# Kernel optimization log

Hardware: AMD Instinct MI355X
Metric: run time of the kernel (lower is better)

## Reference

```python
import jax, jax.numpy as jnp
import numpy as np

D_MODEL = 1024
NHEAD = 16
HEAD_DIM = D_MODEL // NHEAD
D_FF = 4096
B, S = 2, 2048
LN_EPS = 1e-5


def _linear_params(key, d_out, d_in):
    kw, kb = jax.random.split(key)
    lim = 1.0 / np.sqrt(d_in)
    W = jax.random.uniform(kw, (d_out, d_in), jnp.float32, -lim, lim)
    b = jax.random.uniform(kb, (d_out,), jnp.float32, -lim, lim)
    return W, b


def setup_inputs() -> dict:
    key = jax.random.key(0)
    ks = jax.random.split(key, 8)
    src = jax.random.normal(ks[0], (B, S, D_MODEL), jnp.float32)
    mask = jax.random.randint(ks[1], (B, S), 0, 2).astype(bool)
    Wq, bq = _linear_params(ks[2], D_MODEL, D_MODEL)
    Wk, bk = _linear_params(ks[3], D_MODEL, D_MODEL)
    Wv, bv = _linear_params(ks[4], D_MODEL, D_MODEL)
    Wo, bo = _linear_params(ks[5], D_MODEL, D_MODEL)
    W1, b1 = _linear_params(ks[6], D_FF, D_MODEL)
    W2, b2 = _linear_params(ks[7], D_MODEL, D_FF)
    ln1_g = jnp.ones((D_MODEL,), jnp.float32)
    ln1_b = jnp.zeros((D_MODEL,), jnp.float32)
    ln2_g = jnp.ones((D_MODEL,), jnp.float32)
    ln2_b = jnp.zeros((D_MODEL,), jnp.float32)
    return dict(src=src, mask=mask, Wq=Wq, bq=bq, Wk=Wk, bk=bk, Wv=Wv, bv=bv,
                Wo=Wo, bo=bo, W1=W1, b1=b1, W2=W2, b2=b2,
                ln1_g=ln1_g, ln1_b=ln1_b, ln2_g=ln2_g, ln2_b=ln2_b)


def _layernorm(x, g, b):
    mu = jnp.mean(x, axis=-1, keepdims=True)
    var = jnp.mean(jnp.square(x - mu), axis=-1, keepdims=True)
    return (x - mu) * jax.lax.rsqrt(var + LN_EPS) * g + b


def reference(src, mask, Wq, bq, Wk, bk, Wv, bv, Wo, bo, W1, b1, W2, b2,
              ln1_g, ln1_b, ln2_g, ln2_b):
    batch, seq, _ = src.shape
    src_norm = _layernorm(src, ln1_g, ln1_b)
    # projections (torch Linear: x @ W.T + b), split heads -> [B,H,S,Dh]
    def proj(W, b):
        y = jnp.einsum('bsi,oi->bso', src_norm, W) + b
        return y.reshape(batch, seq, NHEAD, HEAD_DIM).transpose(0, 2, 1, 3)
    q, k, v = proj(Wq, bq), proj(Wk, bk), proj(Wv, bv)
    scores = jnp.einsum('bhqd,bhkd->bhqk', q, k) / np.sqrt(HEAD_DIM)
    scores = jnp.where(mask[:, None, None, :], -10000.0, scores)
    attn_probs = jax.nn.softmax(scores, axis=-1)
    attn_out = jnp.einsum('bhqk,bhkd->bhqd', attn_probs, v)
    attn_out = attn_out.transpose(0, 2, 1, 3).reshape(batch, seq, D_MODEL)
    attn_out = jnp.einsum('bsi,oi->bso', attn_out, Wo) + bo
    src = src + attn_out
    src_norm2 = _layernorm(src, ln2_g, ln2_b)
    h = jax.nn.relu(jnp.einsum('bsi,oi->bso', src_norm2, W1) + b1)
    ff = jnp.einsum('bsi,oi->bso', h, W2) + b2
    src = src + ff
    return (src, attn_probs)
```

## Files before the change

kernel.cpp:

```cpp
#include <hip/hip_runtime.h>
#include <math.h>

typedef __bf16 bf16;
typedef __bf16 bf16x4 __attribute__((ext_vector_type(4)));
typedef __bf16 bf16x8 __attribute__((ext_vector_type(8)));
typedef float f32x4 __attribute__((ext_vector_type(4)));

__device__ __forceinline__ f32x4 mfma16(bf16x8 a, bf16x8 b, f32x4 c) {
  return __builtin_amdgcn_mfma_f32_16x16x32_bf16(a, b, c, 0, 0, 0);
}

__device__ __forceinline__ void gload_lds16(const void* g, void* l) {
  __builtin_amdgcn_global_load_lds((__attribute__((address_space(1))) void*)(g),
                                   (__attribute__((address_space(3))) void*)(l),
                                   16, 0, 0);
}

__global__ __launch_bounds__(256)
void prep(const float* __restrict__ Wq, const float* __restrict__ Wk,
          const float* __restrict__ Wv, const float* __restrict__ Wo,
          const float* __restrict__ W1, const float* __restrict__ W2,
          const float* __restrict__ bq, const float* __restrict__ bk,
          const float* __restrict__ bv, bf16* __restrict__ wqkv,
          bf16* __restrict__ wob, bf16* __restrict__ w1b,
          bf16* __restrict__ w2b, float* __restrict__ bqkv,
          const float* __restrict__ src, const float* __restrict__ g,
          const float* __restrict__ bta, bf16* __restrict__ y) {
  __shared__ float red[8];
  if (blockIdx.x < 12291) {
    const int i = blockIdx.x * 256 + threadIdx.x;
    if (i < 3145728) {
      float4 v;
      bf16* dst;
      size_t di;
      if (i < 262144) { v = ((const float4*)Wq)[i]; dst = wqkv; di = i; }
      else if (i < 524288) { v = ((const float4*)Wk)[i - 262144]; dst = wqkv; di = i; }
      else if (i < 786432) { v = ((const float4*)Wv)[i - 524288]; dst = wqkv; di = i; }
      else if (i < 1048576) { v = ((const float4*)Wo)[i - 786432]; dst = wob; di = i - 786432; }
      else if (i < 2097152) { v = ((const float4*)W1)[i - 1048576]; dst = w1b; di = i - 1048576; }
      else { v = ((const float4*)W2)[i - 2097152]; dst = w2b; di = i - 2097152; }
      bf16x4 o;
      o[0] = (bf16)v.x; o[1] = (bf16)v.y; o[2] = (bf16)v.z; o[3] = (bf16)v.w;
      reinterpret_cast<bf16x4*>(dst)[di] = o;
    } else {
      const int j = i - 3145728;
      const float* s = (j < 256) ? bq : ((j < 512) ? bk : bv);
      reinterpret_cast<float4*>(bqkv)[j] = reinterpret_cast<const float4*>(s)[j & 255];
    }
  } else {
    const int row = blockIdx.x - 12291, t = threadIdx.x;
    const float4 v = reinterpret_cast<const float4*>(src)[(size_t)row * 256 + t];
    float s1 = v.x + v.y + v.z + v.w;
    float s2 = v.x * v.x + v.y * v.y + v.z * v.z + v.w * v.w;
#pragma unroll
    for (int m = 1; m < 64; m <<= 1) {
      s1 += __shfl_xor(s1, m);
      s2 += __shfl_xor(s2, m);
    }
    if ((t & 63) == 0) { red[(t >> 6) * 2] = s1; red[(t >> 6) * 2 + 1] = s2; }
    __syncthreads();
    s1 = red[0] + red[2] + red[4] + red[6];
    s2 = red[1] + red[3] + red[5] + red[7];
    const float mu = s1 * (1.f / 1024.f);
    const float rs = rsqrtf(s2 * (1.f / 1024.f) - mu * mu + 1e-5f);
    const float4 gv = reinterpret_cast<const float4*>(g)[t];
    const float4 bv = reinterpret_cast<const float4*>(bta)[t];
    bf16x4 o;
    o[0] = (bf16)((v.x - mu) * rs * gv.x + bv.x);
    o[1] = (bf16)((v.y - mu) * rs * gv.y + bv.y);
    o[2] = (bf16)((v.z - mu) * rs * gv.z + bv.z);
    o[3] = (bf16)((v.w - mu) * rs * gv.w + bv.w);
    reinterpret_cast<bf16x4*>(y)[(size_t)row * 256 + t] = o;
  }
}

__global__ __launch_bounds__(256)
void ln_bf(const bf16* __restrict__ xx, const float* __restrict__ g,
           const float* __restrict__ bta, bf16* __restrict__ y) {
  const int row = blockIdx.x, t = threadIdx.x;
  bf16x4 bv4 = reinterpret_cast<const bf16x4*>(xx)[(size_t)row * 256 + t];
  float4 v;
  v.x = (float)bv4[0]; v.y = (float)bv4[1]; v.z = (float)bv4[2]; v.w = (float)bv4[3];
  float s1 = v.x + v.y + v.z + v.w;
  float s2 = v.x * v.x + v.y * v.y + v.z * v.z + v.w * v.w;
#pragma unroll
  for (int m = 1; m < 64; m <<= 1) {
    s1 += __shfl_xor(s1, m);
    s2 += __shfl_xor(s2, m);
  }
  __shared__ float red[8];
  if ((t & 63) == 0) { red[(t >> 6) * 2] = s1; red[(t >> 6) * 2 + 1] = s2; }
  __syncthreads();
  s1 = red[0] + red[2] + red[4] + red[6];
  s2 = red[1] + red[3] + red[5] + red[7];
  const float mu = s1 * (1.f / 1024.f);
  const float rs = rsqrtf(s2 * (1.f / 1024.f) - mu * mu + 1e-5f);
  const float4 gv = reinterpret_cast<const float4*>(g)[t];
  const float4 bv = reinterpret_cast<const float4*>(bta)[t];
  bf16x4 o;
  o[0] = (bf16)((v.x - mu) * rs * gv.x + bv.x);
  o[1] = (bf16)((v.y - mu) * rs * gv.y + bv.y);
  o[2] = (bf16)((v.z - mu) * rs * gv.z + bv.z);
  o[3] = (bf16)((v.w - mu) * rs * gv.w + bv.w);
  reinterpret_cast<bf16x4*>(y)[(size_t)row * 256 + t] = o;
}

__global__ __launch_bounds__(256)
void tr_v(const bf16* __restrict__ QKV, bf16* __restrict__ VT) {
  __shared__ bf16 T[64 * 80];
  const int t = threadIdx.x;
  const int sb = blockIdx.x * 64, h = blockIdx.y, b = blockIdx.z;
  const int srow = t >> 2, c16 = t & 3;
  const bf16* src = QKV + (size_t)(b * 2048 + sb + srow) * 3072 + 2048 + h * 64 + c16 * 16;
  bf16x8 a0 = *reinterpret_cast<const bf16x8*>(src);
  bf16x8 a1 = *reinterpret_cast<const bf16x8*>(src + 8);
  *reinterpret_cast<bf16x8*>(&T[srow * 80 + c16 * 16]) = a0;
  *reinterpret_cast<bf16x8*>(&T[srow * 80 + c16 * 16 + 8]) = a1;
  __syncthreads();
  const int drow = t >> 2, sq = t & 3;
  bf16x8 o0, o1;
#pragma unroll
  for (int j = 0; j < 8; ++j) o0[j] = T[(sq * 16 + j) * 80 + drow];
#pragma unroll
  for (int j = 0; j < 8; ++j) o1[j] = T[(sq * 16 + 8 + j) * 80 + drow];
  bf16* dst = VT + ((size_t)(b * 16 + h) * 64 + drow) * 2048 + sb + sq * 16;
  *reinterpret_cast<bf16x8*>(dst) = o0;
  *reinterpret_cast<bf16x8*>(dst + 8) = o1;
}

template <bool RELU, bool QSC>
__global__ __launch_bounds__(512)
void gemm_bt3(const bf16* __restrict__ A, const bf16* __restrict__ Bw,
              const float* __restrict__ bias, bf16* __restrict__ Cout,
              int M, int N, int K) {
  __shared__ bf16 As[3][128 * 32];
  __shared__ bf16 Bs[3][256 * 32];
  const int t = threadIdx.x, wave = t >> 6, lane = t & 63;
  const int l15 = lane & 15, lhi = lane >> 4;
  const int nwg = gridDim.x * gridDim.y;
  const int orig = blockIdx.y * gridDim.x + blockIdx.x;
  const int wgid = (orig & 7) * (nwg >> 3) + (orig >> 3);
  const int bx = wgid % gridDim.x, by = wgid / gridDim.x;
  const int m0 = by * 128, n0 = bx * 256;
  const int wm = (wave >> 2) * 64, wn = (wave & 3) * 64;
  const f32x4 z4 = {0.f, 0.f, 0.f, 0.f};
  f32x4 acc[4][4];
#pragma unroll
  for (int m = 0; m < 4; ++m)
#pragma unroll
    for (int n = 0; n < 4; ++n) acc[m][n] = z4;

  const int da = t * 16;
  const int ra = da >> 6, ca = (da & 63) ^ ((ra & 3) << 4);
  const bf16* agp = A + (size_t)(m0 + ra) * K + (ca >> 1);
  int db_[2];
  const bf16* bgp[2];
#pragma unroll
  for (int j = 0; j < 2; ++j) {
    db_[j] = j * 8192 + t * 16;
    const int rb = db_[j] >> 6;
    const int cb = (db_[j] & 63) ^ ((rb & 3) << 4);
    bgp[j] = Bw + (size_t)(n0 + rb) * K + (cb >> 1);
  }

#define G3_STAGE(k0, bb)                                                      \
  do {                                                                        \
    gload_lds16(agp + (k0), (char*)As[bb] + da);                              \
    gload_lds16(bgp[0] + (k0), (char*)Bs[bb] + db_[0]);                       \
    gload_lds16(bgp[1] + (k0), (char*)Bs[bb] + db_[1]);                       \
  } while (0)

  const int nt = K >> 5;
  G3_STAGE(0, 0);
  G3_STAGE(32, 1);
  asm volatile("s_waitcnt vmcnt(3)" ::: "memory");
  __builtin_amdgcn_s_barrier();

  for (int kt = 0; kt < nt; ++kt) {
    if (kt + 2 < nt) G3_STAGE((kt + 2) * 32, (kt + 2) % 3);
    const char* Ac = (const char*)As[kt % 3];
    const char* Bc = (const char*)Bs[kt % 3];
    bf16x8 af[4], bfr[4];
#pragma unroll
    for (int m = 0; m < 4; ++m) {
      const int row = wm + m * 16 + l15;
      af[m] = *reinterpret_cast<const bf16x8*>(
          Ac + row * 64 + ((lhi * 16) ^ ((row & 3) << 4)));
    }
#pragma unroll
    for (int n = 0; n < 4; ++n) {
      const int row = wn + n * 16 + l15;
      bfr[n] = *reinterpret_cast<const bf16x8*>(
          Bc + row * 64 + ((lhi * 16) ^ ((row & 3) << 4)));
    }
    __builtin_amdgcn_s_setprio(1);
#pragma unroll
    for (int m = 0; m < 4; ++m)
#pragma unroll
      for (int n = 0; n < 4; ++n) acc[m][n] = mfma16(af[m], bfr[n], acc[m][n]);
    __builtin_amdgcn_s_setprio(0);
    if (kt + 1 < nt) {
      if (kt + 2 < nt)
        asm volatile("s_waitcnt vmcnt(3)" ::: "memory");
      else
        asm volatile("s_waitcnt vmcnt(0)" ::: "memory");
      __builtin_amdgcn_s_barrier();
    }
  }
#undef G3_STAGE

  const float sc = (QSC && n0 < 1024) ? 0.18033688011112042f : 1.0f;
#pragma unroll
  for (int m = 0; m < 4; ++m) {
    const int row_base = m0 + wm + m * 16 + lhi * 4;
#pragma unroll
    for (int n = 0; n < 4; ++n) {
      const int col = n0 + wn + n * 16 + l15;
      const float bv = bias[col];
#pragma unroll
      for (int r = 0; r < 4; ++r) {
        float v = (acc[m][n][r] + bv) * sc;
        if (RELU) v = v > 0.f ? v : 0.f;
        Cout[(size_t)(row_base + r) * N + col] = (bf16)v;
      }
    }
  }
}

template <bool OUT_BF16, bool RES, bool RESBF>
__global__ __launch_bounds__(256)
void gemm_bt(const bf16* __restrict__ A, const bf16* __restrict__ Bw,
             const float* __restrict__ bias, const void* __restrict__ res,
             void* __restrict__ Cout, int M, int N, int K) {
  __shared__ bf16 As[3][64 * 32];
  __shared__ bf16 Bs[3][128 * 32];
  const int t = threadIdx.x, wave = t >> 6, lane = t & 63;
  const int l15 = lane & 15, lhi = lane >> 4;
  const int nwg = gridDim.x * gridDim.y;
  const int orig = blockIdx.y * gridDim.x + blockIdx.x;
  const int wgid = (orig & 7) * (nwg >> 3) + (orig >> 3);
  const int bx = wgid % gridDim.x, by = wgid / gridDim.x;
  const int m0 = by * 64, n0 = bx * 128;
  const int wm = (wave >> 1) * 32, wn = (wave & 1) * 64;
  const f32x4 z4 = {0.f, 0.f, 0.f, 0.f};
  f32x4 acc[2][4];
#pragma unroll
  for (int m = 0; m < 2; ++m)
#pragma unroll
    for (int n = 0; n < 4; ++n) acc[m][n] = z4;

  int soff[2], srow[2], scol[2];
#pragma unroll
  for (int i = 0; i < 2; ++i) {
    soff[i] = (i * 4 + wave) * 1024 + lane * 16;
    srow[i] = soff[i] >> 6;
    scol[i] = (soff[i] & 63) >> 1;
  }

#define GEMM_STAGE(k0, bb)                                                    \
  do {                                                                        \
    gload_lds16(A + (size_t)(m0 + srow[0]) * K + (k0) + scol[0],              \
                (char*)As[bb] + soff[0]);                                     \
    gload_lds16(Bw + (size_t)(n0 + srow[0]) * K + (k0) + scol[0],             \
                (char*)Bs[bb] + soff[0]);                                     \
    gload_lds16(Bw + (size_t)(n0 + srow[1]) * K + (k0) + scol[1],             \
                (char*)Bs[bb] + soff[1]);                                     \
  } while (0)

  const int nt = K >> 5;
  GEMM_STAGE(0, 0);
  GEMM_STAGE(32, 1);
  asm volatile("s_waitcnt vmcnt(3)" ::: "memory");
  __builtin_amdgcn_s_barrier();

  for (int kt = 0; kt < nt; ++kt) {
    if (kt + 2 < nt) GEMM_STAGE((kt + 2) * 32, (kt + 2) % 3);
    const bf16* Ac = As[kt % 3];
    const bf16* Bc = Bs[kt % 3];
    bf16x8 af[2], bfr[4];
#pragma unroll
    for (int m = 0; m < 2; ++m)
      af[m] = *reinterpret_cast<const bf16x8*>(&Ac[(wm + m * 16 + l15) * 32 + lhi * 8]);
#pragma unroll
    for (int n = 0; n < 4; ++n)
      bfr[n] = *reinterpret_cast<const bf16x8*>(&Bc[(wn + n * 16 + l15) * 32 + lhi * 8]);
    __builtin_amdgcn_s_setprio(1);
#pragma unroll
    for (int m = 0; m < 2; ++m)
#pragma unroll
      for (int n = 0; n < 4; ++n) acc[m][n] = mfma16(af[m], bfr[n], acc[m][n]);
    __builtin_amdgcn_s_setprio(0);
    if (kt + 1 < nt) {
      if (kt + 2 < nt)
        asm volatile("s_waitcnt vmcnt(3)" ::: "memory");
      else
        asm volatile("s_waitcnt vmcnt(0)" ::: "memory");
      __builtin_amdgcn_s_barrier();
    }
  }
#undef GEMM_STAGE

#pragma unroll
  for (int m = 0; m < 2; ++m) {
    const int row_base = m0 + wm + m * 16 + lhi * 4;
#pragma unroll
    for (int n = 0; n < 4; ++n) {
      const int col = n0 + wn + n * 16 + l15;
      const float bv = bias[col];
#pragma unroll
      for (int r = 0; r < 4; ++r) {
        const int row = row_base + r;
        float v = acc[m][n][r] + bv;
        if (RES) {
          const size_t idx = (size_t)row * N + col;
          v += RESBF ? (float)((const bf16*)res)[idx] : ((const float*)res)[idx];
        }
        if (OUT_BF16)
          ((bf16*)Cout)[(size_t)row * N + col] = (bf16)v;
        else
          ((float*)Cout)[(size_t)row * N + col] = v;
      }
    }
  }
}

__global__ __launch_bounds__(512)
void attn_fused2(const bf16* __restrict__ Qp, const bf16* __restrict__ Kp,
                 const bf16* __restrict__ VTp, const int* __restrict__ mask,
                 float* __restrict__ probs, bf16* __restrict__ Ob) {
  constexpr int S = 2048, LD = 3072, KB = 128, NT = S / KB;
  __shared__ bf16 Kt[KB * 64];
  __shared__ bf16 Vt[64 * KB];
  __shared__ bf16 P[128 * KB];
  __shared__ float msk2[2][KB];
  const int t = threadIdx.x, wave = t >> 6, lane = t & 63;
  const int l15 = lane & 15, lhi = lane >> 4;
  const int flat = blockIdx.x + 16 * (blockIdx.y + 16 * blockIdx.z);
  const int wg = (flat & 7) * 64 + (flat >> 3);
  const int q0 = (wg & 15) * 128, h = (wg >> 4) & 15, b = wg >> 8;
  const int* mrow = mask + b * S;
  const f32x4 z4 = {0.f, 0.f, 0.f, 0.f};

  const bf16* kgp[2];
  const bf16* vgp[2];
  int soff[2];
#pragma unroll
  for (int i = 0; i < 2; ++i) {
    const int off = (i * 8 + wave) * 1024 + lane * 16;
    soff[i] = off;
    const int krow = off >> 7, kbin = off & 127;
    kgp[i] = Kp + (size_t)(b * S + krow) * LD + h * 64 + ((kbin ^ ((krow & 7) << 4)) >> 1);
    const int d = off >> 8, vbin = off & 255;
    vgp[i] = VTp + (size_t)((b * 16 + h) * 64 + d) * S + ((vbin ^ ((d & 7) << 4)) >> 1);
  }

  bf16x8 qf[2];
#pragma unroll
  for (int ks = 0; ks < 2; ++ks)
    qf[ks] = *reinterpret_cast<const bf16x8*>(
        Qp + (size_t)(b * S + q0 + wave * 16 + l15) * LD + h * 64 + ks * 32 + lhi * 8);

  bf16x8 kreg[2];
  float mnext;
#pragma unroll
  for (int i = 0; i < 2; ++i) kreg[i] = *reinterpret_cast<const bf16x8*>(kgp[i]);
  mnext = (t < KB) ? (mrow[t] ? 0.f : 1.f) : 0.f;
#pragma unroll
  for (int i = 0; i < 2; ++i)
    *reinterpret_cast<bf16x8*>((char*)Kt + soff[i]) = kreg[i];
  if (t < KB) msk2[0][t] = mnext;
  __syncthreads();

  float lpart = 0.f;
  for (int kt = 0; kt < NT; ++kt) {
    const int kv0 = kt * KB;
    if (kt + 1 < NT) {
#pragma unroll
      for (int i = 0; i < 2; ++i)
        kreg[i] = *reinterpret_cast<const bf16x8*>(kgp[i] + (size_t)(kv0 + KB) * LD);
      mnext = (t < KB) ? (mrow[kv0 + KB + t] ? 0.f : 1.f) : 0.f;
    }
    const char* kb = (kt & 1) ? (const char*)Vt : (const char*)Kt;
    const float* mc = msk2[kt & 1];
    f32x4 sa[8];
#pragma unroll
    for (int n = 0; n < 8; ++n) sa[n] = z4;
    __builtin_amdgcn_s_setprio(1);
#pragma unroll
    for (int ks = 0; ks < 2; ++ks)
#pragma unroll
      for (int n = 0; n < 8; ++n) {
        const int krow = n * 16 + l15;
        bf16x8 kf = *reinterpret_cast<const bf16x8*>(
            kb + krow * 128 + ((ks * 64 + lhi * 16) ^ ((krow & 7) << 4)));
        sa[n] = mfma16(kf, qf[ks], sa[n]);
      }
    __builtin_amdgcn_s_setprio(0);
#pragma unroll
    for (int n = 0; n < 8; ++n)
#pragma unroll
      for (int r = 0; r < 4; ++r)
        lpart += __builtin_exp2f(sa[n][r]) * mc[n * 16 + lhi * 4 + r];
    if (kt + 1 < NT) {
      char* kbn = ((kt + 1) & 1) ? (char*)Vt : (char*)Kt;
#pragma unroll
      for (int i = 0; i < 2; ++i)
        *reinterpret_cast<bf16x8*>(kbn + soff[i]) = kreg[i];
      if (t < KB) msk2[(kt + 1) & 1][t] = mnext;
    }
    __syncthreads();
  }
  lpart += __shfl_xor(lpart, 16);
  lpart += __shfl_xor(lpart, 32);
  const float il = 1.f / lpart;

  f32x4 oa[4];
#pragma unroll
  for (int n = 0; n < 4; ++n) oa[n] = z4;
  float* pbase = probs + ((size_t)(b * 16 + h) * S + q0 + wave * 16 + l15) * S;
  const int prw = wave * 16 + l15;

  bf16x8 vreg[2];
#pragma unroll
  for (int i = 0; i < 2; ++i) {
    kreg[i] = *reinterpret_cast<const bf16x8*>(kgp[i]);
    vreg[i] = *reinterpret_cast<const bf16x8*>(vgp[i]);
  }
  mnext = (t < KB) ? (mrow[t] ? 0.f : 1.f) : 0.f;
#pragma unroll
  for (int i = 0; i < 2; ++i) {
    *reinterpret_cast<bf16x8*>((char*)Kt + soff[i]) = kreg[i];
    *reinterpret_cast<bf16x8*>((char*)Vt + soff[i]) = vreg[i];
  }
  if (t < KB) msk2[0][t] = mnext;
  __syncthreads();

  for (int kt = 0; kt < NT; ++kt) {
    const int kv0 = kt * KB;
    if (kt + 1 < NT) {
#pragma unroll
      for (int i = 0; i < 2; ++i) {
        kreg[i] = *reinterpret_cast<const bf16x8*>(kgp[i] + (size_t)(kv0 + KB) * LD);
        vreg[i] = *reinterpret_cast<const bf16x8*>(vgp[i] + kv0 + KB);
      }
      mnext = (t < KB) ? (mrow[kv0 + KB + t] ? 0.f : 1.f) : 0.f;
    }

    f32x4 sa[8];
#pragma unroll
    for (int n = 0; n < 8; ++n) sa[n] = z4;
    __builtin_amdgcn_s_setprio(1);
#pragma unroll
    for (int ks = 0; ks < 2; ++ks)
#pragma unroll
      for (int n = 0; n < 8; ++n) {
        const int krow = n * 16 + l15;
        bf16x8 kf = *reinterpret_cast<const bf16x8*>(
            (char*)Kt + krow * 128 + ((ks * 64 + lhi * 16) ^ ((krow & 7) << 4)));
        sa[n] = mfma16(kf, qf[ks], sa[n]);
      }
    __builtin_amdgcn_s_setprio(0);

#pragma unroll
    for (int n = 0; n < 8; ++n) {
      f32x4 praw, pn;
#pragma unroll
      for (int r = 0; r < 4; ++r) {
        praw[r] = __builtin_exp2f(sa[n][r]) * msk2[0][n * 16 + lhi * 4 + r];
        pn[r] = praw[r] * il;
      }
      __builtin_nontemporal_store(pn, reinterpret_cast<f32x4*>(pbase + kv0 + n * 16 + lhi * 4));
      bf16x4 pb;
      pb[0] = (bf16)praw[0]; pb[1] = (bf16)praw[1];
      pb[2] = (bf16)praw[2]; pb[3] = (bf16)praw[3];
      *reinterpret_cast<bf16x4*>(
          (char*)P + prw * 256 + ((n * 32 + lhi * 8) ^ ((prw & 7) << 4))) = pb;
    }
    __builtin_amdgcn_s_setprio(1);
#pragma unroll
    for (int ks = 0; ks < 4; ++ks) {
      bf16x8 pf = *reinterpret_cast<const bf16x8*>(
          (char*)P + prw * 256 + ((ks * 64 + lhi * 16) ^ ((prw & 7) << 4)));
#pragma unroll
      for (int nn = 0; nn < 4; ++nn) {
        const int vr = nn * 16 + l15;
        bf16x8 vf = *reinterpret_cast<const bf16x8*>(
            (char*)Vt + vr * 256 + ((ks * 64 + lhi * 16) ^ ((vr & 7) << 4)));
        oa[nn] = mfma16(pf, vf, oa[nn]);
      }
    }
    __builtin_amdgcn_s_setprio(0);
    __syncthreads();
    if (kt + 1 < NT) {
#pragma unroll
      for (int i = 0; i < 2; ++i) {
        *reinterpret_cast<bf16x8*>((char*)Kt + soff[i]) = kreg[i];
        *reinterpret_cast<bf16x8*>((char*)Vt + soff[i]) = vreg[i];
      }
      if (t < KB) msk2[0][t] = mnext;
    }
    __syncthreads();
  }

  float il4[4];
#pragma unroll
  for (int r = 0; r < 4; ++r) il4[r] = __shfl(il, lhi * 4 + r);
#pragma unroll
  for (int nn = 0; nn < 4; ++nn)
#pragma unroll
    for (int r = 0; r < 4; ++r)
      Ob[(size_t)(b * S + q0 + wave * 16 + lhi * 4 + r) * 1024 + h * 64 + nn * 16 + l15] =
          (bf16)(oa[nn][r] * il4[r]);
}

extern "C" void kernel_launch(void* const* d_in, const int* in_sizes, int n_in,
                              void* d_out, int out_size, void* d_ws, size_t ws_size,
                              hipStream_t stream) {
  const float* src = (const float*)d_in[0];
  const int* mask = (const int*)d_in[1];
  const float* Wq = (const float*)d_in[2];
  const float* bq = (const float*)d_in[3];
  const float* Wk = (const float*)d_in[4];
  const float* bk = (const float*)d_in[5];
  const float* Wv = (const float*)d_in[6];
  const float* bv = (const float*)d_in[7];
  const float* Wo = (const float*)d_in[8];
  const float* bo = (const float*)d_in[9];
  const float* W1 = (const float*)d_in[10];
  const float* b1 = (const float*)d_in[11];
  const float* W2 = (const float*)d_in[12];
  const float* b2 = (const float*)d_in[13];
  const float* ln1g = (const float*)d_in[14];
  const float* ln1b = (const float*)d_in[15];
  const float* ln2g = (const float*)d_in[16];
  const float* ln2b = (const float*)d_in[17];

  float* out0 = (float*)d_out;
  float* probs = (float*)d_out + (size_t)4194304;

  char* w = (char*)d_ws;
  const size_t MB = 1u << 20;
  bf16* wqkv = (bf16*)(w);
  bf16* wob = (bf16*)(w + 6 * MB);
  bf16* w1b = (bf16*)(w + 8 * MB);
  bf16* w2b = (bf16*)(w + 16 * MB);
  bf16* xn = (bf16*)(w + 24 * MB);
  bf16* QKV = (bf16*)(w + 32 * MB);
  bf16* Ob = (bf16*)(w + 56 * MB);
  bf16* hb = (bf16*)(w + 32 * MB);
  bf16* VT = (bf16*)(w + 64 * MB);
  bf16* s2 = (bf16*)(w + 72 * MB);
  float* bqkv = (float*)(w + 80 * MB);

  prep<<<16387, 256, 0, stream>>>(Wq, Wk, Wv, Wo, W1, W2, bq, bk, bv,
                                  wqkv, wob, w1b, w2b, bqkv,
                                  src, ln1g, ln1b, xn);
  gemm_bt3<false, true><<<dim3(12, 32), 512, 0, stream>>>(
      xn, wqkv, bqkv, QKV, 4096, 3072, 1024);
  tr_v<<<dim3(32, 16, 2), 256, 0, stream>>>(QKV, VT);
  attn_fused2<<<dim3(16, 16, 2), 512, 0, stream>>>(
      QKV, QKV + 1024, VT, mask, probs, Ob);
  gemm_bt<true, true, false><<<dim3(8, 64), 256, 0, stream>>>(
      Ob, wob, bo, src, s2, 4096, 1024, 1024);
  ln_bf<<<4096, 256, 0, stream>>>(s2, ln2g, ln2b, xn);
  gemm_bt3<true, false><<<dim3(16, 32), 512, 0, stream>>>(
      xn, w1b, b1, hb, 4096, 4096, 1024);
  gemm_bt<false, true, true><<<dim3(8, 64), 256, 0, stream>>>(
      hb, w2b, b2, s2, out0, 4096, 1024, 4096);

  (void)in_sizes; (void)n_in; (void)out_size; (void)ws_size;
}
```

Measured before the change: 405.1 us.

## Fuse V transpose into QKV GEMM epilogue and retile attention for double-buffering

The QKV projection GEMM now writes the V columns directly in transposed head-major layout, which removes the separate tr_v kernel launch and its extra read and write of V. The attention kernel moves to a single shared LDS buffer. The row-sum pass double-buffers K tiles of 128. The probability/PV pass uses 64-key tiles with double-buffered K and V, so one barrier per iteration is dropped. The trade-offs are scattered 8-byte transposed stores in the GEMM epilogue and more loop iterations with smaller MFMA batches per tile.

```diff
diff --git a/kernel.cpp b/kernel.cpp
--- a/kernel.cpp
+++ b/kernel.cpp
@@ -105,34 +105,11 @@
   reinterpret_cast<bf16x4*>(y)[(size_t)row * 256 + t] = o;
 }
 
-__global__ __launch_bounds__(256)
-void tr_v(const bf16* __restrict__ QKV, bf16* __restrict__ VT) {
-  __shared__ bf16 T[64 * 80];
-  const int t = threadIdx.x;
-  const int sb = blockIdx.x * 64, h = blockIdx.y, b = blockIdx.z;
-  const int srow = t >> 2, c16 = t & 3;
-  const bf16* src = QKV + (size_t)(b * 2048 + sb + srow) * 3072 + 2048 + h * 64 + c16 * 16;
-  bf16x8 a0 = *reinterpret_cast<const bf16x8*>(src);
-  bf16x8 a1 = *reinterpret_cast<const bf16x8*>(src + 8);
-  *reinterpret_cast<bf16x8*>(&T[srow * 80 + c16 * 16]) = a0;
-  *reinterpret_cast<bf16x8*>(&T[srow * 80 + c16 * 16 + 8]) = a1;
-  __syncthreads();
-  const int drow = t >> 2, sq = t & 3;
-  bf16x8 o0, o1;
-#pragma unroll
-  for (int j = 0; j < 8; ++j) o0[j] = T[(sq * 16 + j) * 80 + drow];
-#pragma unroll
-  for (int j = 0; j < 8; ++j) o1[j] = T[(sq * 16 + 8 + j) * 80 + drow];
-  bf16* dst = VT + ((size_t)(b * 16 + h) * 64 + drow) * 2048 + sb + sq * 16;
-  *reinterpret_cast<bf16x8*>(dst) = o0;
-  *reinterpret_cast<bf16x8*>(dst + 8) = o1;
-}
-
-template <bool RELU, bool QSC>
+template <bool RELU, bool QSC, bool VTW>
 __global__ __launch_bounds__(512)
 void gemm_bt3(const bf16* __restrict__ A, const bf16* __restrict__ Bw,
               const float* __restrict__ bias, bf16* __restrict__ Cout,
-              int M, int N, int K) {
+              bf16* __restrict__ VTo, int M, int N, int K) {
   __shared__ bf16 As[3][128 * 32];
   __shared__ bf16 Bs[3][256 * 32];
   const int t = threadIdx.x, wave = t >> 6, lane = t & 63;
@@ -217,11 +194,21 @@
     for (int n = 0; n < 4; ++n) {
       const int col = n0 + wn + n * 16 + l15;
       const float bv = bias[col];
-#pragma unroll
-      for (int r = 0; r < 4; ++r) {
-        float v = (acc[m][n][r] + bv) * sc;
-        if (RELU) v = v > 0.f ? v : 0.f;
-        Cout[(size_t)(row_base + r) * N + col] = (bf16)v;
+      if (VTW && col >= 2048) {
+        const int hd = col - 2048, hh = hd >> 6, d = hd & 63;
+        const int bb = row_base >> 11, s = row_base & 2047;
+        bf16x4 vv;
+#pragma unroll
+        for (int r = 0; r < 4; ++r) vv[r] = (bf16)(acc[m][n][r] + bv);
+        *reinterpret_cast<bf16x4*>(
+            VTo + ((size_t)((bb * 16 + hh) * 64 + d) * 2048 + s)) = vv;
+      } else {
+#pragma unroll
+        for (int r = 0; r < 4; ++r) {
+          float v = (acc[m][n][r] + bv) * sc;
+          if (RELU) v = v > 0.f ? v : 0.f;
+          Cout[(size_t)(row_base + r) * N + col] = (bf16)v;
+        }
       }
     }
   }
@@ -328,11 +315,8 @@
 void attn_fused2(const bf16* __restrict__ Qp, const bf16* __restrict__ Kp,
                  const bf16* __restrict__ VTp, const int* __restrict__ mask,
                  float* __restrict__ probs, bf16* __restrict__ Ob) {
-  constexpr int S = 2048, LD = 3072, KB = 128, NT = S / KB;
-  __shared__ bf16 Kt[KB * 64];
-  __shared__ bf16 Vt[64 * KB];
-  __shared__ bf16 P[128 * KB];
-  __shared__ float msk2[2][KB];
+  constexpr int S = 2048, LD = 3072;
+  __shared__ char lds[50176];
   const int t = threadIdx.x, wave = t >> 6, lane = t & 63;
   const int l15 = lane & 15, lhi = lane >> 4;
   const int flat = blockIdx.x + 16 * (blockIdx.y + 16 * blockIdx.z);
@@ -340,18 +324,16 @@
   const int q0 = (wg & 15) * 128, h = (wg >> 4) & 15, b = wg >> 8;
   const int* mrow = mask + b * S;
   const f32x4 z4 = {0.f, 0.f, 0.f, 0.f};
-
-  const bf16* kgp[2];
-  const bf16* vgp[2];
-  int soff[2];
+  float* mskA = (float*)(lds + 49152);
+
+  const bf16* kgpA[2];
+  int soffA[2];
 #pragma unroll
   for (int i = 0; i < 2; ++i) {
     const int off = (i * 8 + wave) * 1024 + lane * 16;
-    soff[i] = off;
+    soffA[i] = off;
     const int krow = off >> 7, kbin = off & 127;
-    kgp[i] = Kp + (size_t)(b * S + krow) * LD + h * 64 + ((kbin ^ ((krow & 7) << 4)) >> 1);
-    const int d = off >> 8, vbin = off & 255;
-    vgp[i] = VTp + (size_t)((b * 16 + h) * 64 + d) * S + ((vbin ^ ((d & 7) << 4)) >> 1);
+    kgpA[i] = Kp + (size_t)(b * S + krow) * LD + h * 64 + ((kbin ^ ((krow & 7) << 4)) >> 1);
   }
 
   bf16x8 qf[2];
@@ -363,141 +345,140 @@
   bf16x8 kreg[2];
   float mnext;
 #pragma unroll
-  for (int i = 0; i < 2; ++i) kreg[i] = *reinterpret_cast<const bf16x8*>(kgp[i]);
-  mnext = (t < KB) ? (mrow[t] ? 0.f : 1.f) : 0.f;
+  for (int i = 0; i < 2; ++i) kreg[i] = *reinterpret_cast<const bf16x8*>(kgpA[i]);
+  mnext = (t < 128) ? (mrow[t] ? 0.f : 1.f) : 0.f;
 #pragma unroll
   for (int i = 0; i < 2; ++i)
-    *reinterpret_cast<bf16x8*>((char*)Kt + soff[i]) = kreg[i];
-  if (t < KB) msk2[0][t] = mnext;
+    *reinterpret_cast<bf16x8*>(lds + soffA[i]) = kreg[i];
+  if (t < 128) mskA[t] = mnext;
   __syncthreads();
 
   float lpart = 0.f;
-  for (int kt = 0; kt < NT; ++kt) {
-    const int kv0 = kt * KB;
-    if (kt + 1 < NT) {
+  for (int kt = 0; kt < 16; ++kt) {
+    const int kv0 = kt * 128;
+    if (kt + 1 < 16) {
 #pragma unroll
       for (int i = 0; i < 2; ++i)
-        kreg[i] = *reinterpret_cast<const bf16x8*>(kgp[i] + (size_t)(kv0 + KB) * LD);
-      mnext = (t < KB) ? (mrow[kv0 + KB + t] ? 0.f : 1.f) : 0.f;
-    }
-    const char* kb = (kt & 1) ? (const char*)Vt : (const char*)Kt;
-    const float* mc = msk2[kt & 1];
-    f32x4 sa[8];
-#pragma unroll
-    for (int n = 0; n < 8; ++n) sa[n] = z4;
+        kreg[i] = *reinterpret_cast<const bf16x8*>(kgpA[i] + (size_t)(kv0 + 128) * LD);
+      mnext = (t < 128) ? (mrow[kv0 + 128 + t] ? 0.f : 1.f) : 0.f;
+    }
+    const char* kb = lds + (kt & 1) * 16384;
+    const float* mc = mskA + (kt & 1) * 128;
+#pragma unroll
+    for (int g = 0; g < 2; ++g) {
+      f32x4 sa[4];
+#pragma unroll
+      for (int n = 0; n < 4; ++n) sa[n] = z4;
+      __builtin_amdgcn_s_setprio(1);
+#pragma unroll
+      for (int ks = 0; ks < 2; ++ks)
+#pragma unroll
+        for (int n = 0; n < 4; ++n) {
+          const int krow = g * 64 + n * 16 + l15;
+          bf16x8 kf = *reinterpret_cast<const bf16x8*>(
+              kb + krow * 128 + ((ks * 64 + lhi * 16) ^ ((krow & 7) << 4)));
+          sa[n] = mfma16(kf, qf[ks], sa[n]);
+        }
+      __builtin_amdgcn_s_setprio(0);
+#pragma unroll
+      for (int n = 0; n < 4; ++n)
+#pragma unroll
+        for (int r = 0; r < 4; ++r)
+          lpart += __builtin_exp2f(sa[n][r]) * mc[g * 64 + n * 16 + lhi * 4 + r];
+    }
+    if (kt + 1 < 16) {
+      char* kbn = lds + ((kt + 1) & 1) * 16384;
+#pragma unroll
+      for (int i = 0; i < 2; ++i)
+        *reinterpret_cast<bf16x8*>(kbn + soffA[i]) = kreg[i];
+      if (t < 128) mskA[((kt + 1) & 1) * 128 + t] = mnext;
+    }
+    __syncthreads();
+  }
+  lpart += __shfl_xor(lpart, 16);
+  lpart += __shfl_xor(lpart, 32);
+  const float il = 1.f / lpart;
+
+  const int offB = t * 16;
+  const int krB = offB >> 7, binB = offB & 127;
+  const int swB = (binB ^ ((krB & 7) << 4)) >> 1;
+  const bf16* kgpB = Kp + (size_t)(b * S + krB) * LD + h * 64 + swB;
+  const bf16* vgpB = VTp + (size_t)((b * 16 + h) * 64 + krB) * S + swB;
+  char* Pb = lds + 32768;
+
+  f32x4 oa[4];
+#pragma unroll
+  for (int n = 0; n < 4; ++n) oa[n] = z4;
+  float* pbase = probs + ((size_t)(b * 16 + h) * S + q0 + wave * 16 + l15) * S;
+  const int prw = wave * 16 + l15;
+  const int swzp = (prw & 7) << 4;
+
+  bf16x8 krg = *reinterpret_cast<const bf16x8*>(kgpB);
+  bf16x8 vrg = *reinterpret_cast<const bf16x8*>(vgpB);
+  mnext = (t < 64) ? (mrow[t] ? 0.f : 1.f) : 0.f;
+  *reinterpret_cast<bf16x8*>(lds + offB) = krg;
+  *reinterpret_cast<bf16x8*>(lds + 16384 + offB) = vrg;
+  if (t < 64) mskA[t] = mnext;
+  __syncthreads();
+
+  for (int kt = 0; kt < 32; ++kt) {
+    const int kv0 = kt * 64;
+    if (kt + 1 < 32) {
+      krg = *reinterpret_cast<const bf16x8*>(kgpB + (size_t)(kv0 + 64) * LD);
+      vrg = *reinterpret_cast<const bf16x8*>(vgpB + kv0 + 64);
+      mnext = (t < 64) ? (mrow[kv0 + 64 + t] ? 0.f : 1.f) : 0.f;
+    }
+    const char* kc = lds + (kt & 1) * 8192;
+    const char* vc = lds + 16384 + (kt & 1) * 8192;
+    const float* mc = mskA + (kt & 1) * 64;
+
+    f32x4 sa[4];
+#pragma unroll
+    for (int n = 0; n < 4; ++n) sa[n] = z4;
     __builtin_amdgcn_s_setprio(1);
 #pragma unroll
     for (int ks = 0; ks < 2; ++ks)
 #pragma unroll
-      for (int n = 0; n < 8; ++n) {
+      for (int n = 0; n < 4; ++n) {
         const int krow = n * 16 + l15;
         bf16x8 kf = *reinterpret_cast<const bf16x8*>(
-            kb + krow * 128 + ((ks * 64 + lhi * 16) ^ ((krow & 7) << 4)));
+            kc + krow * 128 + ((ks * 64 + lhi * 16) ^ ((krow & 7) << 4)));
         sa[n] = mfma16(kf, qf[ks], sa[n]);
       }
     __builtin_amdgcn_s_setprio(0);
-#pragma unroll
-    for (int n = 0; n < 8; ++n)
-#pragma unroll
-      for (int r = 0; r < 4; ++r)
-        lpart += __builtin_exp2f(sa[n][r]) * mc[n * 16 + lhi * 4 + r];
-    if (kt + 1 < NT) {
-      char* kbn = ((kt + 1) & 1) ? (char*)Vt : (char*)Kt;
-#pragma unroll
-      for (int i = 0; i < 2; ++i)
-        *reinterpret_cast<bf16x8*>(kbn + soff[i]) = kreg[i];
-      if (t < KB) msk2[(kt + 1) & 1][t] = mnext;
-    }
-    __syncthreads();
-  }
-  lpart += __shfl_xor(lpart, 16);
-  lpart += __shfl_xor(lpart, 32);
-  const float il = 1.f / lpart;
-
-  f32x4 oa[4];
-#pragma unroll
-  for (int n = 0; n < 4; ++n) oa[n] = z4;
-  float* pbase = probs + ((size_t)(b * 16 + h) * S + q0 + wave * 16 + l15) * S;
-  const int prw = wave * 16 + l15;
-
-  bf16x8 vreg[2];
-#pragma unroll
-  for (int i = 0; i < 2; ++i) {
-    kreg[i] = *reinterpret_cast<const bf16x8*>(kgp[i]);
-    vreg[i] = *reinterpret_cast<const bf16x8*>(vgp[i]);
-  }
-  mnext = (t < KB) ? (mrow[t] ? 0.f : 1.f) : 0.f;
-#pragma unroll
-  for (int i = 0; i < 2; ++i) {
-    *reinterpret_cast<bf16x8*>((char*)Kt + soff[i]) = kreg[i];
-    *reinterpret_cast<bf16x8*>((char*)Vt + soff[i]) = vreg[i];
-  }
-  if (t < KB) msk2[0][t] = mnext;
-  __syncthreads();
-
-  for (int kt = 0; kt < NT; ++kt) {
-    const int kv0 = kt * KB;
-    if (kt + 1 < NT) {
-#pragma unroll
-      for (int i = 0; i < 2; ++i) {
-        kreg[i] = *reinterpret_cast<const bf16x8*>(kgp[i] + (size_t)(kv0 + KB) * LD);
-        vreg[i] = *reinterpret_cast<const bf16x8*>(vgp[i] + kv0 + KB);
-      }
-      mnext = (t < KB) ? (mrow[kv0 + KB + t] ? 0.f : 1.f) : 0.f;
-    }
-
-    f32x4 sa[8];
-#pragma unroll
-    for (int n = 0; n < 8; ++n) sa[n] = z4;
-    __builtin_amdgcn_s_setprio(1);
-#pragma unroll
-    for (int ks = 0; ks < 2; ++ks)
-#pragma unroll
-      for (int n = 0; n < 8; ++n) {
-        const int krow = n * 16 + l15;
-        bf16x8 kf = *reinterpret_cast<const bf16x8*>(
-            (char*)Kt + krow * 128 + ((ks * 64 + lhi * 16) ^ ((krow & 7) << 4)));
-        sa[n] = mfma16(kf, qf[ks], sa[n]);
-      }
-    __builtin_amdgcn_s_setprio(0);
-
-#pragma unroll
-    for (int n = 0; n < 8; ++n) {
+
+#pragma unroll
+    for (int n = 0; n < 4; ++n) {
       f32x4 praw, pn;
 #pragma unroll
       for (int r = 0; r < 4; ++r) {
-        praw[r] = __builtin_exp2f(sa[n][r]) * msk2[0][n * 16 + lhi * 4 + r];
+        praw[r] = __builtin_exp2f(sa[n][r]) * mc[n * 16 + lhi * 4 + r];
         pn[r] = praw[r] * il;
       }
       __builtin_nontemporal_store(pn, reinterpret_cast<f32x4*>(pbase + kv0 + n * 16 + lhi * 4));
       bf16x4 pb;
       pb[0] = (bf16)praw[0]; pb[1] = (bf16)praw[1];
       pb[2] = (bf16)praw[2]; pb[3] = (bf16)praw[3];
-      *reinterpret_cast<bf16x4*>(
-          (char*)P + prw * 256 + ((n * 32 + lhi * 8) ^ ((prw & 7) << 4))) = pb;
+      *reinterpret_cast<bf16x4*>(Pb + prw * 128 + ((n * 32 + lhi * 8) ^ swzp)) = pb;
     }
     __builtin_amdgcn_s_setprio(1);
 #pragma unroll
-    for (int ks = 0; ks < 4; ++ks) {
+    for (int ks = 0; ks < 2; ++ks) {
       bf16x8 pf = *reinterpret_cast<const bf16x8*>(
-          (char*)P + prw * 256 + ((ks * 64 + lhi * 16) ^ ((prw & 7) << 4)));
+          Pb + prw * 128 + ((ks * 64 + lhi * 16) ^ swzp));
 #pragma unroll
       for (int nn = 0; nn < 4; ++nn) {
         const int vr = nn * 16 + l15;
         bf16x8 vf = *reinterpret_cast<const bf16x8*>(
-            (char*)Vt + vr * 256 + ((ks * 64 + lhi * 16) ^ ((vr & 7) << 4)));
+            vc + vr * 128 + ((ks * 64 + lhi * 16) ^ ((vr & 7) << 4)));
         oa[nn] = mfma16(pf, vf, oa[nn]);
       }
     }
     __builtin_amdgcn_s_setprio(0);
-    __syncthreads();
-    if (kt + 1 < NT) {
-#pragma unroll
-      for (int i = 0; i < 2; ++i) {
-        *reinterpret_cast<bf16x8*>((char*)Kt + soff[i]) = kreg[i];
-        *reinterpret_cast<bf16x8*>((char*)Vt + soff[i]) = vreg[i];
-      }
-      if (t < KB) msk2[0][t] = mnext;
+    if (kt + 1 < 32) {
+      *reinterpret_cast<bf16x8*>(lds + ((kt + 1) & 1) * 8192 + offB) = krg;
+      *reinterpret_cast<bf16x8*>(lds + 16384 + ((kt + 1) & 1) * 8192 + offB) = vrg;
+      if (t < 64) mskA[((kt + 1) & 1) * 64 + t] = mnext;
     }
     __syncthreads();
   }
@@ -555,16 +536,15 @@
   prep<<<16387, 256, 0, stream>>>(Wq, Wk, Wv, Wo, W1, W2, bq, bk, bv,
                                   wqkv, wob, w1b, w2b, bqkv,
                                   src, ln1g, ln1b, xn);
-  gemm_bt3<false, true><<<dim3(12, 32), 512, 0, stream>>>(
-      xn, wqkv, bqkv, QKV, 4096, 3072, 1024);
-  tr_v<<<dim3(32, 16, 2), 256, 0, stream>>>(QKV, VT);
+  gemm_bt3<false, true, true><<<dim3(12, 32), 512, 0, stream>>>(
+      xn, wqkv, bqkv, QKV, VT, 4096, 3072, 1024);
   attn_fused2<<<dim3(16, 16, 2), 512, 0, stream>>>(
       QKV, QKV + 1024, VT, mask, probs, Ob);
   gemm_bt<true, true, false><<<dim3(8, 64), 256, 0, stream>>>(
       Ob, wob, bo, src, s2, 4096, 1024, 1024);
   ln_bf<<<4096, 256, 0, stream>>>(s2, ln2g, ln2b, xn);
-  gemm_bt3<true, false><<<dim3(16, 32), 512, 0, stream>>>(
-      xn, w1b, b1, hb, 4096, 4096, 1024);
+  gemm_bt3<true, false, false><<<dim3(16, 32), 512, 0, stream>>>(
+      xn, w1b, b1, hb, nullptr, 4096, 4096, 1024);
   gemm_bt<false, true, true><<<dim3(8, 64), 256, 0, stream>>>(
       hb, w2b, b2, s2, out0, 4096, 1024, 4096);
 
```

Measured after the change: 399.2 us. No clear change (-1.5%).
